# Kernel tuning notes

Measured on AMD Instinct MI355X. Metric: run time of the kernel, lower is better.

Reference implementation:

```python
import jax, jax.numpy as jnp
import numpy as np

H = 512
L = 4096
LOC_CNT = 100000


def setup_inputs() -> dict:
    key = jax.random.key(0)
    ks = jax.random.split(key, 12)
    stdv = 1.0 / np.sqrt(H)

    def unif(k, shape):
        return jax.random.uniform(k, shape, dtype=jnp.float32, minval=-stdv, maxval=stdv)

    return {
        "td_upper": jax.random.uniform(ks[0], (L,), dtype=jnp.float32),
        "td_lower": jax.random.uniform(ks[1], (L,), dtype=jnp.float32),
        "ld_upper": jax.random.uniform(ks[2], (L,), dtype=jnp.float32),
        "ld_lower": jax.random.uniform(ks[3], (L,), dtype=jnp.float32),
        "loc": jax.random.randint(ks[4], (L,), 0, LOC_CNT, dtype=jnp.int64),
        "hx": jax.random.normal(ks[5], (H, 1), dtype=jnp.float32),
        "W_ih": unif(ks[6], (H, H)),
        "W_th_upper": unif(ks[7], (H, H)),
        "W_th_lower": unif(ks[8], (H, H)),
        "W_sh_upper": unif(ks[9], (H, H)),
        "W_sh_lower": unif(ks[10], (H, H)),
        "loc_table": unif(ks[11], (LOC_CNT, H)),
    }


def reference(td_upper, td_lower, ld_upper, ld_lower, loc, hx,
              W_ih, W_th_upper, W_th_lower, W_sh_upper, W_sh_lower, loc_table):
    # Gather location embeddings: (L, H)
    emb = loc_table[loc]
    # Ttd[i] @ emb[i] where Ttd[i] = (W_tu*tu_i + W_tl*tl_i)/(tu_i+tl_i):
    # distribute the scalar-weighted combine over the matmul.
    a = emb @ W_th_upper.T            # (L, H) == (W_th_upper @ emb[i])^T per row
    b = emb @ W_th_lower.T
    v = (a * td_upper[:, None] + b * td_lower[:, None]) / (td_upper + td_lower)[:, None]
    # Sld[i] @ v[i]
    c = v @ W_sh_upper.T
    d = v @ W_sh_lower.T
    w = (c * ld_upper[:, None] + d * ld_lower[:, None]) / (ld_upper + ld_lower)[:, None]
    # Original: torch.sum(torch.cat(...)) -> full scalar reduction over all L*H values.
    loc_vec = jnp.sum(w)
    usr_vec = W_ih @ hx               # (H, 1)
    return jax.nn.sigmoid(loc_vec + usr_vec)
```

## Files before the change

### kernel.cpp

```cpp
#include <hip/hip_runtime.h>
#include <math.h>

namespace {

constexpr int H = 512;
constexpr int L = 4096;

constexpr int WS_SU  = 0;
constexpr int WS_SL  = 512;
constexpr int WS_G   = 1024;
constexpr int WS_IHV = 3072;
constexpr int WS_ACC = 3584;
constexpr int WS_TOT = 3585;

constexpr int GB = 256;
constexpr int CB = 128;
constexpr int WB = 8;

__device__ inline float wave_reduce(float v) {
#pragma unroll
    for (int off = 32; off; off >>= 1) v += __shfl_xor(v, off, 64);
    return v;
}

__global__ __launch_bounds__(512) void stageA_k(
    const float* __restrict__ tu, const float* __restrict__ tl,
    const float* __restrict__ lu, const float* __restrict__ ll,
    const int* __restrict__ loc, const float* __restrict__ table,
    const float* __restrict__ Wsu, const float* __restrict__ Wsl,
    const float* __restrict__ Wih, const float* __restrict__ hx,
    float* __restrict__ ws) {
    const int b = blockIdx.x;
    const int t = threadIdx.x;
    if (b < GB) {
        float aa = 0.f, ab = 0.f, ag = 0.f, ad = 0.f;
        const int row0 = b * (L / GB);
#pragma unroll
        for (int r = 0; r < L / GB; ++r) {
            const int row = row0 + r;
            const float tuv = tu[row], tlv = tl[row];
            const float luv = lu[row], llv = ll[row];
            const float ti = 1.f / (tuv + tlv), li = 1.f / (luv + llv);
            const float Tu = tuv * ti, Tl = tlv * ti;
            const float Lu = luv * li, Ll = llv * li;
            const float e = table[(size_t)loc[row] * H + t];
            aa += Lu * Tu * e;
            ab += Lu * Tl * e;
            ag += Ll * Tu * e;
            ad += Ll * Tl * e;
        }
        atomicAdd(ws + WS_G + 0 * H + t, aa);
        atomicAdd(ws + WS_G + 1 * H + t, ab);
        atomicAdd(ws + WS_G + 2 * H + t, ag);
        atomicAdd(ws + WS_G + 3 * H + t, ad);
    } else if (b < GB + CB) {
        const int cb = b - GB;
        const int mat = cb >> 6;
        const int m0 = (cb & 63) * (H / 64);
        const float* W = mat ? Wsl : Wsu;
        float acc = 0.f;
#pragma unroll
        for (int r = 0; r < H / 64; ++r) acc += W[(size_t)(m0 + r) * H + t];
        atomicAdd(ws + (mat ? WS_SL : WS_SU) + t, acc);
    } else {
        const int wb = b - GB - CB;
        const int lane = t & 63, wid = t >> 6;
        const int j = lane * 8;
        const float4 xA = *reinterpret_cast<const float4*>(hx + j);
        const float4 xB = *reinterpret_cast<const float4*>(hx + j + 4);
#pragma unroll
        for (int r = 0; r < 8; ++r) {
            const int row = wb * 64 + wid * 8 + r;
            const float4 wA = *reinterpret_cast<const float4*>(Wih + (size_t)row * H + j);
            const float4 wB = *reinterpret_cast<const float4*>(Wih + (size_t)row * H + j + 4);
            float a = wA.x * xA.x + wA.y * xA.y + wA.z * xA.z + wA.w * xA.w
                    + wB.x * xB.x + wB.y * xB.y + wB.z * xB.z + wB.w * xB.w;
            a = wave_reduce(a);
            if (lane == 0) ws[WS_IHV + row] = a;
        }
    }
}

__global__ __launch_bounds__(512) void stageB_k(
    const float* __restrict__ Wtu, const float* __restrict__ Wtl,
    float* __restrict__ ws) {
    const int t = threadIdx.x;
    const int lane = t & 63, wid = t >> 6;
    const int gw = blockIdx.x * 8 + wid;
    const int mat = gw >> 9;
    const int h = gw & (H - 1);
    const float* W = mat ? Wtl : Wtu;
    const float* g1 = ws + WS_G + (mat ? 1 : 0) * H;
    const float* g2 = ws + WS_G + (mat ? 3 : 2) * H;
    const float suh = ws[WS_SU + h], slh = ws[WS_SL + h];
    const int j = lane * 8;
    const float4 wA = *reinterpret_cast<const float4*>(W + (size_t)h * H + j);
    const float4 wB = *reinterpret_cast<const float4*>(W + (size_t)h * H + j + 4);
    const float4 aA = *reinterpret_cast<const float4*>(g1 + j);
    const float4 aB = *reinterpret_cast<const float4*>(g1 + j + 4);
    const float4 bA = *reinterpret_cast<const float4*>(g2 + j);
    const float4 bB = *reinterpret_cast<const float4*>(g2 + j + 4);
    float acc = wA.x * (suh * aA.x + slh * bA.x)
              + wA.y * (suh * aA.y + slh * bA.y)
              + wA.z * (suh * aA.z + slh * bA.z)
              + wA.w * (suh * aA.w + slh * bA.w)
              + wB.x * (suh * aB.x + slh * bB.x)
              + wB.y * (suh * aB.y + slh * bB.y)
              + wB.z * (suh * aB.z + slh * bB.z)
              + wB.w * (suh * aB.w + slh * bB.w);
    acc = wave_reduce(acc);
    if (lane == 0) atomicAdd(ws + WS_ACC, acc);
}

__global__ __launch_bounds__(512) void stageC_k(
    const float* __restrict__ ws, float* __restrict__ out) {
    const int t = threadIdx.x;
    const float x = ws[WS_ACC] + ws[WS_IHV + t];
    out[t] = 1.f / (1.f + expf(-x));
}

}

extern "C" void kernel_launch(void* const* d_in, const int* in_sizes, int n_in,
                              void* d_out, int out_size, void* d_ws, size_t ws_size,
                              hipStream_t stream) {
    const float* tu    = (const float*)d_in[0];
    const float* tl    = (const float*)d_in[1];
    const float* lu    = (const float*)d_in[2];
    const float* ll    = (const float*)d_in[3];
    const int*   loc   = (const int*)d_in[4];
    const float* hx    = (const float*)d_in[5];
    const float* Wih   = (const float*)d_in[6];
    const float* Wtu   = (const float*)d_in[7];
    const float* Wtl   = (const float*)d_in[8];
    const float* Wsu   = (const float*)d_in[9];
    const float* Wsl   = (const float*)d_in[10];
    const float* table = (const float*)d_in[11];
    float* ws  = (float*)d_ws;
    float* out = (float*)d_out;

    hipMemsetAsync(ws, 0, WS_TOT * sizeof(float), stream);
    stageA_k<<<GB + CB + WB, 512, 0, stream>>>(tu, tl, lu, ll, loc, table,
                                               Wsu, Wsl, Wih, hx, ws);
    stageB_k<<<128, 512, 0, stream>>>(Wtu, Wtl, ws);
    stageC_k<<<1, 512, 0, stream>>>(ws, out);
}
```

Baseline: 285.0 us.

## Replicate atomic accumulators and fuse final sigmoid into stage B via last-block counter

The gather blocks now write into 8 replicated partial-sum buffers, and the column-sum blocks write into 4, which cuts atomic contention on the same addresses. Stage B sums the replicas before its dot products. Stage B also does a block-level reduction before a single atomic per block, and the last block to finish, detected with a counter, applies the sigmoid, which removes the separate stage C launch. The gather work is split into half as many blocks, each handling twice as many rows, so there is less parallelism for the latency-bound table gather.

```diff
diff --git a/kernel.cpp b/kernel.cpp
--- a/kernel.cpp
+++ b/kernel.cpp
@@ -5,17 +5,21 @@
 
 constexpr int H = 512;
 constexpr int L = 4096;
+constexpr int REPG = 8;
+constexpr int REPS = 4;
 
 constexpr int WS_SU  = 0;
-constexpr int WS_SL  = 512;
-constexpr int WS_G   = 1024;
-constexpr int WS_IHV = 3072;
-constexpr int WS_ACC = 3584;
-constexpr int WS_TOT = 3585;
+constexpr int WS_SL  = WS_SU + REPS * H;
+constexpr int WS_G   = WS_SL + REPS * H;
+constexpr int WS_IHV = WS_G + REPG * 4 * H;
+constexpr int WS_ACC = WS_IHV + H;
+constexpr int WS_CNT = WS_ACC + 1;
+constexpr int WS_TOT = WS_CNT + 1;
 
-constexpr int GB = 256;
+constexpr int GB = 128;
 constexpr int CB = 128;
 constexpr int WB = 8;
+constexpr int BGRID = 128;
 
 __device__ inline float wave_reduce(float v) {
 #pragma unroll
@@ -33,9 +37,10 @@
     const int b = blockIdx.x;
     const int t = threadIdx.x;
     if (b < GB) {
+        const int rep = b & (REPG - 1);
         float aa = 0.f, ab = 0.f, ag = 0.f, ad = 0.f;
         const int row0 = b * (L / GB);
-#pragma unroll
+#pragma unroll 16
         for (int r = 0; r < L / GB; ++r) {
             const int row = row0 + r;
             const float tuv = tu[row], tlv = tl[row];
@@ -49,19 +54,22 @@
             ag += Ll * Tu * e;
             ad += Ll * Tl * e;
         }
-        atomicAdd(ws + WS_G + 0 * H + t, aa);
-        atomicAdd(ws + WS_G + 1 * H + t, ab);
-        atomicAdd(ws + WS_G + 2 * H + t, ag);
-        atomicAdd(ws + WS_G + 3 * H + t, ad);
+        float* g = ws + WS_G + rep * (4 * H);
+        atomicAdd(g + 0 * H + t, aa);
+        atomicAdd(g + 1 * H + t, ab);
+        atomicAdd(g + 2 * H + t, ag);
+        atomicAdd(g + 3 * H + t, ad);
     } else if (b < GB + CB) {
         const int cb = b - GB;
         const int mat = cb >> 6;
-        const int m0 = (cb & 63) * (H / 64);
+        const int q = cb & 63;
+        const int m0 = q * (H / 64);
+        const int rep = q & (REPS - 1);
         const float* W = mat ? Wsl : Wsu;
         float acc = 0.f;
 #pragma unroll
         for (int r = 0; r < H / 64; ++r) acc += W[(size_t)(m0 + r) * H + t];
-        atomicAdd(ws + (mat ? WS_SL : WS_SU) + t, acc);
+        atomicAdd(ws + (mat ? WS_SL : WS_SU) + rep * H + t, acc);
     } else {
         const int wb = b - GB - CB;
         const int lane = t & 63, wid = t >> 6;
@@ -83,40 +91,73 @@
 
 __global__ __launch_bounds__(512) void stageB_k(
     const float* __restrict__ Wtu, const float* __restrict__ Wtl,
-    float* __restrict__ ws) {
+    float* __restrict__ ws, float* __restrict__ out) {
     const int t = threadIdx.x;
     const int lane = t & 63, wid = t >> 6;
     const int gw = blockIdx.x * 8 + wid;
     const int mat = gw >> 9;
     const int h = gw & (H - 1);
     const float* W = mat ? Wtl : Wtu;
-    const float* g1 = ws + WS_G + (mat ? 1 : 0) * H;
-    const float* g2 = ws + WS_G + (mat ? 3 : 2) * H;
-    const float suh = ws[WS_SU + h], slh = ws[WS_SL + h];
+    const int v1 = mat ? 1 : 0;
+    const int v2 = mat ? 3 : 2;
+
+    float suh = 0.f, slh = 0.f;
+#pragma unroll
+    for (int rp = 0; rp < REPS; ++rp) {
+        suh += ws[WS_SU + rp * H + h];
+        slh += ws[WS_SL + rp * H + h];
+    }
+
     const int j = lane * 8;
+    float a1[8] = {0, 0, 0, 0, 0, 0, 0, 0};
+    float a2[8] = {0, 0, 0, 0, 0, 0, 0, 0};
+#pragma unroll
+    for (int rp = 0; rp < REPG; ++rp) {
+        const float* g1 = ws + WS_G + (rp * 4 + v1) * H + j;
+        const float* g2 = ws + WS_G + (rp * 4 + v2) * H + j;
+        const float4 x0 = *reinterpret_cast<const float4*>(g1);
+        const float4 x1 = *reinterpret_cast<const float4*>(g1 + 4);
+        const float4 y0 = *reinterpret_cast<const float4*>(g2);
+        const float4 y1 = *reinterpret_cast<const float4*>(g2 + 4);
+        a1[0] += x0.x; a1[1] += x0.y; a1[2] += x0.z; a1[3] += x0.w;
+        a1[4] += x1.x; a1[5] += x1.y; a1[6] += x1.z; a1[7] += x1.w;
+        a2[0] += y0.x; a2[1] += y0.y; a2[2] += y0.z; a2[3] += y0.w;
+        a2[4] += y1.x; a2[5] += y1.y; a2[6] += y1.z; a2[7] += y1.w;
+    }
+
     const float4 wA = *reinterpret_cast<const float4*>(W + (size_t)h * H + j);
     const float4 wB = *reinterpret_cast<const float4*>(W + (size_t)h * H + j + 4);
-    const float4 aA = *reinterpret_cast<const float4*>(g1 + j);
-    const float4 aB = *reinterpret_cast<const float4*>(g1 + j + 4);
-    const float4 bA = *reinterpret_cast<const float4*>(g2 + j);
-    const float4 bB = *reinterpret_cast<const float4*>(g2 + j + 4);
-    float acc = wA.x * (suh * aA.x + slh * bA.x)
-              + wA.y * (suh * aA.y + slh * bA.y)
-              + wA.z * (suh * aA.z + slh * bA.z)
-              + wA.w * (suh * aA.w + slh * bA.w)
-              + wB.x * (suh * aB.x + slh * bB.x)
-              + wB.y * (suh * aB.y + slh * bB.y)
-              + wB.z * (suh * aB.z + slh * bB.z)
-              + wB.w * (suh * aB.w + slh * bB.w);
+    float acc = wA.x * (suh * a1[0] + slh * a2[0])
+              + wA.y * (suh * a1[1] + slh * a2[1])
+              + wA.z * (suh * a1[2] + slh * a2[2])
+              + wA.w * (suh * a1[3] + slh * a2[3])
+              + wB.x * (suh * a1[4] + slh * a2[4])
+              + wB.y * (suh * a1[5] + slh * a2[5])
+              + wB.z * (suh * a1[6] + slh * a2[6])
+              + wB.w * (suh * a1[7] + slh * a2[7]);
     acc = wave_reduce(acc);
-    if (lane == 0) atomicAdd(ws + WS_ACC, acc);
-}
 
-__global__ __launch_bounds__(512) void stageC_k(
-    const float* __restrict__ ws, float* __restrict__ out) {
-    const int t = threadIdx.x;
-    const float x = ws[WS_ACC] + ws[WS_IHV + t];
-    out[t] = 1.f / (1.f + expf(-x));
+    __shared__ float wp[8];
+    __shared__ float accs;
+    __shared__ int lastf;
+    if (lane == 0) wp[wid] = acc;
+    __syncthreads();
+    if (t == 0) {
+        float s = 0.f;
+#pragma unroll
+        for (int w = 0; w < 8; ++w) s += wp[w];
+        atomicAdd(ws + WS_ACC, s);
+        __threadfence();
+        const int old = atomicAdd(reinterpret_cast<int*>(ws) + WS_CNT, 1);
+        lastf = (old == (int)gridDim.x - 1) ? 1 : 0;
+    }
+    __syncthreads();
+    if (lastf) {
+        if (t == 0) accs = atomicAdd(ws + WS_ACC, 0.0f);
+        __syncthreads();
+        const float x = accs + ws[WS_IHV + t];
+        out[t] = 1.f / (1.f + expf(-x));
+    }
 }
 
 }
@@ -142,6 +183,5 @@
     hipMemsetAsync(ws, 0, WS_TOT * sizeof(float), stream);
     stageA_k<<<GB + CB + WB, 512, 0, stream>>>(tu, tl, lu, ll, loc, table,
                                                Wsu, Wsl, Wih, hx, ws);
-    stageB_k<<<128, 512, 0, stream>>>(Wtu, Wtl, ws);
-    stageC_k<<<1, 512, 0, stream>>>(ws, out);
+    stageB_k<<<BGRID, 512, 0, stream>>>(Wtu, Wtl, ws, out);
 }
```

New measurement: 274.6 us. 3.7% less time.
